# Kernel optimization log

Hardware: AMD Instinct MI355X
Metric: run time of the kernel (lower is better)

## Reference

```python
import jax, jax.numpy as jnp
import numpy as np

N = 100000   # nodes
E = 1600000  # edges
B = 256      # graphs
EPS = 1e-5   # batchnorm eps


def setup_inputs() -> dict:
    key = jax.random.key(0)
    ks = jax.random.split(key, 20)
    inp = {
        "x": jax.random.normal(ks[0], (N, 22), dtype=jnp.float32),
        "edge_index": jax.random.randint(ks[1], (2, E), 0, N, dtype=jnp.int64),
        "batch": jnp.sort(jax.random.randint(ks[2], (N,), 0, B, dtype=jnp.int64)),
        # GCNConv weights (x @ W + b convention)
        "W1": jax.random.normal(ks[3], (22, 64), dtype=jnp.float32) * 0.2,
        "b1": jnp.zeros((64,), dtype=jnp.float32),
        "W2": jax.random.normal(ks[4], (64, 64), dtype=jnp.float32) * 0.12,
        "b2": jnp.zeros((64,), dtype=jnp.float32),
        "W3": jax.random.normal(ks[5], (64, 128), dtype=jnp.float32) * 0.12,
        "b3": jnp.zeros((128,), dtype=jnp.float32),
        # BatchNorm1d params + running stats (eval mode)
        "g1": jax.random.uniform(ks[6], (64,), minval=0.5, maxval=1.5),
        "be1": jax.random.normal(ks[7], (64,)) * 0.1,
        "m1": jax.random.normal(ks[8], (64,)) * 0.1,
        "v1": jax.random.uniform(ks[9], (64,), minval=0.5, maxval=1.5),
        "g2": jax.random.uniform(ks[10], (64,), minval=0.5, maxval=1.5),
        "be2": jax.random.normal(ks[11], (64,)) * 0.1,
        "m2": jax.random.normal(ks[12], (64,)) * 0.1,
        "v2": jax.random.uniform(ks[13], (64,), minval=0.5, maxval=1.5),
    }
    return inp


def _gcn_conv(h, W, b, src, dst, norm_e, dinv):
    # PyG GCNConv: h' = D^{-1/2}(A+I)D^{-1/2} (h W) + b
    h = h @ W                                             # [N, F]
    msg = h[src] * norm_e[:, None]                        # gather + scale [E, F]
    agg = jax.ops.segment_sum(msg, dst, num_segments=N)   # scatter-add
    agg = agg + h * dinv[:, None]                         # self-loop term
    return agg + b


def _bn_eval(x, g, be, m, v):
    return (x - m) * jax.lax.rsqrt(v + EPS) * g + be


def reference(x, edge_index, batch, W1, b1, W2, b2, W3, b3,
              g1, be1, m1, v1, g2, be2, m2, v2):
    src, dst = edge_index[0], edge_index[1]
    # degree with self-loops (computed on target nodes, symmetric norm)
    deg = jax.ops.segment_sum(jnp.ones((E,), x.dtype), dst, num_segments=N) + 1.0
    dis = jax.lax.rsqrt(deg)            # deg^{-1/2}, deg >= 1
    norm_e = dis[src] * dis[dst]        # per-edge norm
    dinv = dis * dis                    # 1/deg for self-loop edges

    h = jax.nn.relu(_bn_eval(_gcn_conv(x, W1, b1, src, dst, norm_e, dinv), g1, be1, m1, v1))
    h = jax.nn.relu(_bn_eval(_gcn_conv(h, W2, b2, src, dst, norm_e, dinv), g2, be2, m2, v2))
    h = jax.nn.relu(_gcn_conv(h, W3, b3, src, dst, norm_e, dinv))

    # global mean pool over graph ids
    sums = jax.ops.segment_sum(h, batch, num_segments=B)              # [B, 128]
    cnts = jax.ops.segment_sum(jnp.ones((N,), h.dtype), batch, num_segments=B)
    return sums / jnp.maximum(cnts, 1.0)[:, None]
```

## Files before the change

### kernel.cpp

```cpp
#include <hip/hip_runtime.h>

#define BN_EPS 1e-5f
#define EPB 4096
#define CAP 10240

typedef _Float16 half_t;
typedef _Float16 half4 __attribute__((ext_vector_type(4)));
typedef _Float16 half8 __attribute__((ext_vector_type(8)));
typedef float f32x4 __attribute__((ext_vector_type(4)));
typedef unsigned int u32;
typedef unsigned short u16;

__device__ __forceinline__ float norm_of(u32 w) {
    u16 hb = (u16)(w & 0x7fffu);
    return (float)__builtin_bit_cast(half_t, hb);
}


__global__ void k_front(const float* __restrict__ X, half_t* __restrict__ Xh,
                        const float* __restrict__ W1, const float* __restrict__ b1,
                        const float* __restrict__ g1, const float* __restrict__ be1,
                        const float* __restrict__ m1, const float* __restrict__ v1,
                        const float* __restrict__ W2, const float* __restrict__ b2,
                        const float* __restrict__ g2, const float* __restrict__ be2,
                        const float* __restrict__ m2, const float* __restrict__ v2,
                        const float* __restrict__ W3, const float* __restrict__ b3,
                        half_t* __restrict__ B1h, half_t* __restrict__ B1l,
                        half_t* __restrict__ B2h, half_t* __restrict__ B2l,
                        half_t* __restrict__ B3h, half_t* __restrict__ B3l,
                        float* __restrict__ C1, float* __restrict__ C2,
                        float* __restrict__ C3,
                        int* __restrict__ gcnt, float* __restrict__ sums,
                        int n, int nB) {
    int i = blockIdx.x * 256 + threadIdx.x;
    if (i < 64) {
        float A = g1[i] * rsqrtf(v1[i] + BN_EPS);
        C1[i] = be1[i] + (b1[i] - m1[i]) * A;
    } else if (i < 128) {
        int c = i - 64;
        float A = g2[c] * rsqrtf(v2[c] + BN_EPS);
        C2[c] = be2[c] + (b2[c] - m2[c]) * A;
    } else if (i < 256) {
        int c = i - 128;
        C3[c] = b3[c];
    }
    if (i < 256) gcnt[i] = 0;
    if (i < nB * 128) sums[i] = 0.0f;
    int e = i - 256;
    if (e >= 0 && e < 2048) {
        int j = e & 7, l = (e >> 3) & 63, t = e >> 9;
        int k = ((l >> 4) << 3) + j;
        int col = t * 16 + (l & 15);
        float A = g1[col] * rsqrtf(v1[col] + BN_EPS);
        float w = (k < 22) ? W1[k * 64 + col] * A : 0.0f;
        half_t wh = (half_t)w;
        B1h[e] = wh; B1l[e] = (half_t)(w - (float)wh);
    } else if (e >= 2048 && e < 6144) {
        int e2 = e - 2048;
        int j = e2 & 7, l = (e2 >> 3) & 63, rest = e2 >> 9;
        int s = rest & 1, t = rest >> 1;
        int k = s * 32 + ((l >> 4) << 3) + j;
        int col = t * 16 + (l & 15);
        float A = g2[col] * rsqrtf(v2[col] + BN_EPS);
        float w = W2[k * 64 + col] * A;
        half_t wh = (half_t)w;
        B2h[e2] = wh; B2l[e2] = (half_t)(w - (float)wh);
    } else if (e >= 6144 && e < 14336) {
        int e3 = e - 6144;
        int j = e3 & 7, l = (e3 >> 3) & 63, rest = e3 >> 9;
        int s = rest & 1, t = rest >> 1;
        int k = s * 32 + ((l >> 4) << 3) + j;
        int col = t * 16 + (l & 15);
        float w = W3[k * 128 + col];
        half_t wh = (half_t)w;
        B3h[e3] = wh; B3l[e3] = (half_t)(w - (float)wh);
    }
    if ((long long)i < (long long)n * 24) {
        int node = i / 24, c = i % 24;
        Xh[i] = (c < 22) ? (half_t)X[(size_t)node * 22 + c] : (half_t)0.0f;
    }
}


__global__ __launch_bounds__(256) void k_scatter(const int* __restrict__ src,
                                                 const int* __restrict__ dst,
                                                 int* __restrict__ gcnt,
                                                 u32* __restrict__ rec, int e) {
    __shared__ int h[256];
    __shared__ int cur[256];
    int t = threadIdx.x;
    h[t] = 0;
    __syncthreads();
    int base = blockIdx.x * EPB;
    int end = min(base + EPB, e);
    for (int i = base + t; i < end; i += 256)
        atomicAdd(&h[dst[i] >> 9], 1);
    __syncthreads();
    int c = h[t];
    cur[t] = (c > 0) ? atomicAdd(&gcnt[t], c) : 0;
    __syncthreads();
    for (int i = base + t; i < end; i += 256) {
        int d = dst[i], sv = src[i];
        int bk = d >> 9;
        int pos = atomicAdd(&cur[bk], 1);
        if (pos < CAP)
            rec[(size_t)bk * CAP + pos] = ((u32)sv << 9) | (u32)(d & 511);
    }
}


__global__ __launch_bounds__(256) void k_bmake(const u32* __restrict__ rec,
                                               const int* __restrict__ gcnt,
                                               int2* __restrict__ rp,
                                               float* __restrict__ dis,
                                               float* __restrict__ dinv, int n) {
    __shared__ int h[512];
    __shared__ int ps[256];
    int t = threadIdx.x;
    int b = blockIdx.x;
    int cnt = min(gcnt[b], CAP);
    size_t beg = (size_t)b * CAP;
    h[t] = 0; h[t + 256] = 0;
    __syncthreads();
    for (int i = t; i < cnt; i += 256)
        atomicAdd(&h[rec[beg + i] & 511], 1);
    __syncthreads();
    int d0 = h[2 * t], d1 = h[2 * t + 1];
    int pair = d0 + d1;
    ps[t] = pair;
    __syncthreads();
    int val = pair;
    for (int off = 1; off < 256; off <<= 1) {
        int tmp = (t >= off) ? ps[t - off] : 0;
        __syncthreads();
        val += tmp;
        ps[t] = val;
        __syncthreads();
    }
    int excl = (int)beg + val - pair;
    int node0 = b << 9;
    int nodeA = node0 + 2 * t, nodeB = nodeA + 1;
    if (nodeA < n) {
        rp[nodeA] = make_int2(excl, excl + d0);
        float dd = (float)(d0 + 1);
        dis[nodeA] = rsqrtf(dd);
        dinv[nodeA] = 1.0f / dd;
    }
    if (nodeB < n) {
        rp[nodeB] = make_int2(excl + d0, excl + d0 + d1);
        float dd = (float)(d1 + 1);
        dis[nodeB] = rsqrtf(dd);
        dinv[nodeB] = 1.0f / dd;
    }
}


__global__ __launch_bounds__(256) void k_bfill(const u32* __restrict__ rec,
                                               const int* __restrict__ gcnt,
                                               const int2* __restrict__ rp,
                                               const float* __restrict__ dis,
                                               u32* __restrict__ csr, int n) {
    __shared__ int cur[512];
    __shared__ float disl[512];
    int t = threadIdx.x;
    int b = blockIdx.x;
    int cnt = min(gcnt[b], CAP);
    size_t beg = (size_t)b * CAP;
    int node0 = b << 9;
    for (int j = t; j < 512; j += 256) {
        int node = node0 + j;
        cur[j] = (node < n) ? rp[node].x : 0;
        disl[j] = (node < n) ? dis[node] : 0.0f;
    }
    __syncthreads();
    for (int i = t; i < cnt; i += 256) {
        u32 r = rec[beg + i];
        int dl = r & 511;
        int s = (int)(r >> 9);
        int pos = atomicAdd(&cur[dl], 1);
        half_t hh = (half_t)(dis[s] * disl[dl]);
        csr[pos] = ((u32)s << 15) | (u32)__builtin_bit_cast(u16, hh);
    }
}


__global__ void k_gather22h(const half_t* __restrict__ Xh, const int2* __restrict__ rp,
                            const u32* __restrict__ csr, const float* __restrict__ dinv,
                            half_t* __restrict__ out, int n) {
    int node = blockIdx.x * 4 + (threadIdx.x >> 6);
    if (node >= n) return;
    int lane = threadIdx.x & 63;
    int esub = lane >> 3;
    int sub  = lane & 7;
    bool act = sub < 6;
    const half4* X4 = (const half4*)Xh;
    int2 be = rp[node];
    int beg = be.x, end = be.y;
    float di = dinv[node];
    half4 hs{};
    if (esub == 0 && act) hs = X4[(size_t)node * 6 + sub];
    float4 a0 = make_float4(0, 0, 0, 0), a1 = a0;
    for (int e = beg; e < end; e += 32) {
        int i0 = e + esub, i1 = i0 + 8, i2 = i0 + 16, i3 = i0 + 24;
        u32 w0 = csr[min(i0, end - 1)];
        u32 w1 = csr[min(i1, end - 1)];
        u32 w2 = csr[min(i2, end - 1)];
        u32 w3 = csr[min(i3, end - 1)];
        if (act && i0 < end) {
            float nn = norm_of(w0);
            half4 h = X4[(size_t)(w0 >> 15) * 6 + sub];
            a0.x = fmaf((float)h.x, nn, a0.x); a0.y = fmaf((float)h.y, nn, a0.y);
            a0.z = fmaf((float)h.z, nn, a0.z); a0.w = fmaf((float)h.w, nn, a0.w);
        }
        if (act && i1 < end) {
            float nn = norm_of(w1);
            half4 h = X4[(size_t)(w1 >> 15) * 6 + sub];
            a1.x = fmaf((float)h.x, nn, a1.x); a1.y = fmaf((float)h.y, nn, a1.y);
            a1.z = fmaf((float)h.z, nn, a1.z); a1.w = fmaf((float)h.w, nn, a1.w);
        }
        if (act && i2 < end) {
            float nn = norm_of(w2);
            half4 h = X4[(size_t)(w2 >> 15) * 6 + sub];
            a0.x = fmaf((float)h.x, nn, a0.x); a0.y = fmaf((float)h.y, nn, a0.y);
            a0.z = fmaf((float)h.z, nn, a0.z); a0.w = fmaf((float)h.w, nn, a0.w);
        }
        if (act && i3 < end) {
            float nn = norm_of(w3);
            half4 h = X4[(size_t)(w3 >> 15) * 6 + sub];
            a1.x = fmaf((float)h.x, nn, a1.x); a1.y = fmaf((float)h.y, nn, a1.y);
            a1.z = fmaf((float)h.z, nn, a1.z); a1.w = fmaf((float)h.w, nn, a1.w);
        }
    }
    float4 a;
    a.x = a0.x + a1.x; a.y = a0.y + a1.y; a.z = a0.z + a1.z; a.w = a0.w + a1.w;
#pragma unroll
    for (int d = 8; d <= 32; d <<= 1) {
        a.x += __shfl_xor(a.x, d); a.y += __shfl_xor(a.y, d);
        a.z += __shfl_xor(a.z, d); a.w += __shfl_xor(a.w, d);
    }
    if (esub == 0 && act) {
        half4 r;
        r.x = (half_t)fmaf((float)hs.x, di, a.x);
        r.y = (half_t)fmaf((float)hs.y, di, a.y);
        r.z = (half_t)fmaf((float)hs.z, di, a.z);
        r.w = (half_t)fmaf((float)hs.w, di, a.w);
        ((half4*)out)[(size_t)node * 6 + sub] = r;
    }
}

__global__ void k_gather64h(const half_t* __restrict__ H, const int2* __restrict__ rp,
                            const u32* __restrict__ csr, const float* __restrict__ dinv,
                            half_t* __restrict__ out, int n) {
    int lane = threadIdx.x & 63;
    int nsub = lane >> 5;
    int hl   = lane & 31;
    int esub = hl >> 3;
    int sub  = hl & 7;
    int node = blockIdx.x * 8 + (int)(threadIdx.x >> 6) * 2 + nsub;
    if (node >= n) return;
    const half8* H8 = (const half8*)H;
    int2 be = rp[node];
    int beg = be.x, end = be.y;
    float di = dinv[node];
    half8 hs{};
    if (esub == 0) hs = H8[(size_t)node * 8 + sub];
    float a0[8], a1[8];
#pragma unroll
    for (int j = 0; j < 8; ++j) { a0[j] = 0.0f; a1[j] = 0.0f; }
    for (int e = beg; e < end; e += 16) {
        int i0 = e + esub, i1 = i0 + 4, i2 = i0 + 8, i3 = i0 + 12;
        u32 w0 = csr[min(i0, end - 1)];
        u32 w1 = csr[min(i1, end - 1)];
        u32 w2 = csr[min(i2, end - 1)];
        u32 w3 = csr[min(i3, end - 1)];
        if (i0 < end) {
            float nn = norm_of(w0);
            half8 h = H8[(size_t)(w0 >> 15) * 8 + sub];
#pragma unroll
            for (int j = 0; j < 8; ++j) a0[j] = fmaf((float)h[j], nn, a0[j]);
        }
        if (i1 < end) {
            float nn = norm_of(w1);
            half8 h = H8[(size_t)(w1 >> 15) * 8 + sub];
#pragma unroll
            for (int j = 0; j < 8; ++j) a1[j] = fmaf((float)h[j], nn, a1[j]);
        }
        if (i2 < end) {
            float nn = norm_of(w2);
            half8 h = H8[(size_t)(w2 >> 15) * 8 + sub];
#pragma unroll
            for (int j = 0; j < 8; ++j) a0[j] = fmaf((float)h[j], nn, a0[j]);
        }
        if (i3 < end) {
            float nn = norm_of(w3);
            half8 h = H8[(size_t)(w3 >> 15) * 8 + sub];
#pragma unroll
            for (int j = 0; j < 8; ++j) a1[j] = fmaf((float)h[j], nn, a1[j]);
        }
    }
    float acc[8];
#pragma unroll
    for (int j = 0; j < 8; ++j) acc[j] = a0[j] + a1[j];
#pragma unroll
    for (int d = 8; d <= 16; d <<= 1) {
#pragma unroll
        for (int j = 0; j < 8; ++j) acc[j] += __shfl_xor(acc[j], d);
    }
    if (esub == 0) {
        half8 r;
#pragma unroll
        for (int j = 0; j < 8; ++j) r[j] = (half_t)fmaf((float)hs[j], di, acc[j]);
        ((half8*)out)[(size_t)node * 8 + sub] = r;
    }
}


template <int FIN, int KS, int FOUT>
__global__ __launch_bounds__(256) void k_mgemm(const half_t* __restrict__ P,
                                               const half_t* __restrict__ Bh,
                                               const half_t* __restrict__ Bl,
                                               const float* __restrict__ Cf,
                                               half_t* __restrict__ outp, int n) {
    int lane = threadIdx.x & 63;
    int wv = threadIdx.x >> 6;
    int node0 = blockIdx.x * 64 + wv * 16;
    int arow = lane & 15, kg = lane >> 4;
    int node = node0 + arow;
    bool v = node < n;

    half8 a[KS];
#pragma unroll
    for (int s = 0; s < KS; ++s) {
        bool ld = v && (FIN == 64 || kg < 3);
        a[s] = ld ? *(const half8*)(P + (size_t)node * FIN + s * 32 + kg * 8) : half8{};
    }

    constexpr int NT = FOUT / 16;
    const half8* BH = (const half8*)Bh;
    const half8* BL = (const half8*)Bl;
    int colb = lane & 15;
#pragma unroll
    for (int t = 0; t < NT; ++t) {
        float cinit = Cf[t * 16 + colb];
        f32x4 acc = {cinit, cinit, cinit, cinit};
#pragma unroll
        for (int s = 0; s < KS; ++s) {
            half8 bh = BH[(t * KS + s) * 64 + lane];
            half8 bl = BL[(t * KS + s) * 64 + lane];
            acc = __builtin_amdgcn_mfma_f32_16x16x32_f16(a[s], bh, acc, 0, 0, 0);
            acc = __builtin_amdgcn_mfma_f32_16x16x32_f16(a[s], bl, acc, 0, 0, 0);
        }
#pragma unroll
        for (int r = 0; r < 4; ++r) {
            int nd = node0 + kg * 4 + r;
            if (nd < n)
                outp[(size_t)nd * FOUT + t * 16 + colb] = (half_t)fmaxf(acc[r], 0.0f);
        }
    }
}


__global__ __launch_bounds__(256) void k_mgemm3pool(const half_t* __restrict__ P,
                                                    const half_t* __restrict__ Bh,
                                                    const half_t* __restrict__ Bl,
                                                    const float* __restrict__ Cf,
                                                    const int* __restrict__ batch,
                                                    float* __restrict__ sums, int n) {
    __shared__ half_t tile[128][66];
    __shared__ int batl[64];
    int lane = threadIdx.x & 63;
    int wv = threadIdx.x >> 6;
    int node0 = blockIdx.x * 64 + wv * 16;
    int arow = lane & 15, kg = lane >> 4;
    int node = node0 + arow;
    bool v = node < n;

    if (threadIdx.x < 64) {
        int nd = blockIdx.x * 64 + threadIdx.x;
        batl[threadIdx.x] = (nd < n) ? batch[nd] : -1;
    }

    half8 a[2];
#pragma unroll
    for (int s = 0; s < 2; ++s)
        a[s] = v ? *(const half8*)(P + (size_t)node * 64 + s * 32 + kg * 8) : half8{};

    const half8* BH = (const half8*)Bh;
    const half8* BL = (const half8*)Bl;
    int colb = lane & 15;
#pragma unroll
    for (int t = 0; t < 8; ++t) {
        float cinit = Cf[t * 16 + colb];
        f32x4 acc = {cinit, cinit, cinit, cinit};
#pragma unroll
        for (int s = 0; s < 2; ++s) {
            half8 bh = BH[(t * 2 + s) * 64 + lane];
            half8 bl = BL[(t * 2 + s) * 64 + lane];
            acc = __builtin_amdgcn_mfma_f32_16x16x32_f16(a[s], bh, acc, 0, 0, 0);
            acc = __builtin_amdgcn_mfma_f32_16x16x32_f16(a[s], bl, acc, 0, 0, 0);
        }
#pragma unroll
        for (int r = 0; r < 4; ++r)
            tile[t * 16 + colb][wv * 16 + kg * 4 + r] = (half_t)fmaxf(acc[r], 0.0f);
    }
    __syncthreads();
    if (threadIdx.x < 128) {
        int col = threadIdx.x;
        int cur = batl[0];
        float acc = 0.0f;
        for (int i = 0; i < 64; ++i) {
            int b = batl[i];
            if (b < 0) break;
            if (b != cur) { atomicAdd(&sums[cur * 128 + col], acc); acc = 0.0f; cur = b; }
            acc += (float)tile[col][i];
        }
        if (cur >= 0) atomicAdd(&sums[cur * 128 + col], acc);
    }
}


__global__ void k_pool_div(const float* __restrict__ sums, const int* __restrict__ batch,
                           float* __restrict__ out, int n, int nB) {
    int i = blockIdx.x * blockDim.x + threadIdx.x;
    if (i >= nB * 128) return;
    int b = i >> 7;
    int lo = 0, hi = n;
    while (lo < hi) { int mid = (lo + hi) >> 1; if (batch[mid] < b) lo = mid + 1; else hi = mid; }
    int start = lo;
    lo = 0; hi = n;
    while (lo < hi) { int mid = (lo + hi) >> 1; if (batch[mid] < b + 1) lo = mid + 1; else hi = mid; }
    float cnt = (float)(lo - start);
    out[i] = sums[i] / fmaxf(cnt, 1.0f);
}


extern "C" void kernel_launch(void* const* d_in, const int* in_sizes, int n_in,
                              void* d_out, int out_size, void* d_ws, size_t ws_size,
                              hipStream_t stream) {
    const float* x   = (const float*)d_in[0];
    const int*   ei  = (const int*)d_in[1];
    const int*   bat = (const int*)d_in[2];
    const float* W1  = (const float*)d_in[3];
    const float* b1  = (const float*)d_in[4];
    const float* W2  = (const float*)d_in[5];
    const float* b2  = (const float*)d_in[6];
    const float* W3  = (const float*)d_in[7];
    const float* b3  = (const float*)d_in[8];
    const float* g1  = (const float*)d_in[9];
    const float* be1 = (const float*)d_in[10];
    const float* m1  = (const float*)d_in[11];
    const float* v1  = (const float*)d_in[12];
    const float* g2  = (const float*)d_in[13];
    const float* be2 = (const float*)d_in[14];
    const float* m2  = (const float*)d_in[15];
    const float* v2  = (const float*)d_in[16];

    const int N = in_sizes[0] / 22;
    const int E = in_sizes[1] / 2;
    const int B = out_size / 128;
    const int* src = ei;
    const int* dst = ei + E;

    const int nblk = (E + EPB - 1) / EPB;
    const int NBKT = (N + 511) >> 9;

    size_t off = 0;
    char* base = (char*)d_ws;
    auto alloc = [&](size_t bytes) -> void* {
        void* p = base + off;
        off = (off + bytes + 255) & ~(size_t)255;
        return p;
    };
    int2*   rp     = (int2*)alloc((size_t)N * 8);
    int*    gcnt   = (int*)alloc(256 * 4);
    u32*    rec    = (u32*)alloc((size_t)NBKT * CAP * 4);
    float*  dis    = (float*)alloc((size_t)N * 4);
    float*  dinv   = (float*)alloc((size_t)N * 4);
    u32*    csr    = (u32*)alloc((size_t)NBKT * CAP * 4);
    half_t* Xh     = (half_t*)alloc((size_t)N * 24 * 2);
    half_t* Hh1    = (half_t*)alloc((size_t)N * 64 * 2);
    half_t* Hh2    = (half_t*)alloc((size_t)N * 64 * 2);
    half_t* aggH   = (half_t*)alloc((size_t)N * 64 * 2);
    float*  sums   = (float*)alloc((size_t)B * 128 * 4);
    half_t* B1h    = (half_t*)alloc(2048 * 2);
    half_t* B1l    = (half_t*)alloc(2048 * 2);
    half_t* B2h    = (half_t*)alloc(4096 * 2);
    half_t* B2l    = (half_t*)alloc(4096 * 2);
    half_t* B3h    = (half_t*)alloc(8192 * 2);
    half_t* B3l    = (half_t*)alloc(8192 * 2);
    float*  C1     = (float*)alloc(64 * 4);
    float*  C2     = (float*)alloc(64 * 4);
    float*  C3     = (float*)alloc(128 * 4);

    const int T = 256;
    auto blk = [](long long n, int t) { return (int)((n + t - 1) / t); };

    int gf = blk((long long)N * 24, T);
    int gf2 = blk(256 + 14336, T);
    int gf3 = blk((long long)B * 128, T);
    if (gf2 > gf) gf = gf2;
    if (gf3 > gf) gf = gf3;

    k_front<<<gf, T, 0, stream>>>(x, Xh, W1, b1, g1, be1, m1, v1,
                                  W2, b2, g2, be2, m2, v2, W3, b3,
                                  B1h, B1l, B2h, B2l, B3h, B3l,
                                  C1, C2, C3, gcnt, sums, N, B);

    k_scatter<<<nblk, T, 0, stream>>>(src, dst, gcnt, rec, E);
    k_bmake<<<NBKT, T, 0, stream>>>(rec, gcnt, rp, dis, dinv, N);
    k_bfill<<<NBKT, T, 0, stream>>>(rec, gcnt, rp, dis, csr, N);

    k_gather22h<<<blk(N, 4), T, 0, stream>>>(Xh, rp, csr, dinv, aggH, N);
    k_mgemm<24, 1, 64><<<blk(N, 64), T, 0, stream>>>(aggH, B1h, B1l, C1, Hh1, N);

    k_gather64h<<<blk(N, 8), T, 0, stream>>>(Hh1, rp, csr, dinv, aggH, N);
    k_mgemm<64, 2, 64><<<blk(N, 64), T, 0, stream>>>(aggH, B2h, B2l, C2, Hh2, N);

    k_gather64h<<<blk(N, 8), T, 0, stream>>>(Hh2, rp, csr, dinv, aggH, N);
    k_mgemm3pool<<<blk(N, 64), T, 0, stream>>>(aggH, B3h, B3l, C3, bat, sums, N);

    k_pool_div<<<blk((long long)B * 128, T), T, 0, stream>>>(sums, bat, (float*)d_out, N, B);
}
```

Measured before the change: 292.3 us.

## Use nontemporal loads/stores and one node per wave in 64-wide gather

Streaming accesses to the edge records, CSR and intermediate activations across the scatter, bucket, gather and GEMM kernels now use nontemporal load/store builtins, so that streamed data does not evict the reused feature rows from cache. Separately, k_gather64h changes from two nodes per wave (32 lanes each) to one node per wave with 8 edge subgroups, and the launch grid is adjusted to match. This gives more edge parallelism per node at the cost of more idle lanes for low-degree nodes. Nontemporal stores of data that the next kernel reads right away may hurt if those lines would otherwise have stayed in L2.

```diff
diff --git a/kernel.cpp b/kernel.cpp
--- a/kernel.cpp
+++ b/kernel.cpp
@@ -94,17 +94,19 @@
     int base = blockIdx.x * EPB;
     int end = min(base + EPB, e);
     for (int i = base + t; i < end; i += 256)
-        atomicAdd(&h[dst[i] >> 9], 1);
+        atomicAdd(&h[__builtin_nontemporal_load(&dst[i]) >> 9], 1);
     __syncthreads();
     int c = h[t];
     cur[t] = (c > 0) ? atomicAdd(&gcnt[t], c) : 0;
     __syncthreads();
     for (int i = base + t; i < end; i += 256) {
-        int d = dst[i], sv = src[i];
+        int d = __builtin_nontemporal_load(&dst[i]);
+        int sv = __builtin_nontemporal_load(&src[i]);
         int bk = d >> 9;
         int pos = atomicAdd(&cur[bk], 1);
         if (pos < CAP)
-            rec[(size_t)bk * CAP + pos] = ((u32)sv << 9) | (u32)(d & 511);
+            __builtin_nontemporal_store(((u32)sv << 9) | (u32)(d & 511),
+                                        &rec[(size_t)bk * CAP + pos]);
     }
 }
 
@@ -123,7 +125,7 @@
     h[t] = 0; h[t + 256] = 0;
     __syncthreads();
     for (int i = t; i < cnt; i += 256)
-        atomicAdd(&h[rec[beg + i] & 511], 1);
+        atomicAdd(&h[__builtin_nontemporal_load(&rec[beg + i]) & 511], 1);
     __syncthreads();
     int d0 = h[2 * t], d1 = h[2 * t + 1];
     int pair = d0 + d1;
@@ -174,12 +176,13 @@
     }
     __syncthreads();
     for (int i = t; i < cnt; i += 256) {
-        u32 r = rec[beg + i];
+        u32 r = __builtin_nontemporal_load(&rec[beg + i]);
         int dl = r & 511;
         int s = (int)(r >> 9);
         int pos = atomicAdd(&cur[dl], 1);
         half_t hh = (half_t)(dis[s] * disl[dl]);
-        csr[pos] = ((u32)s << 15) | (u32)__builtin_bit_cast(u16, hh);
+        __builtin_nontemporal_store(((u32)s << 15) | (u32)__builtin_bit_cast(u16, hh),
+                                    &csr[pos]);
     }
 }
 
@@ -202,10 +205,10 @@
     float4 a0 = make_float4(0, 0, 0, 0), a1 = a0;
     for (int e = beg; e < end; e += 32) {
         int i0 = e + esub, i1 = i0 + 8, i2 = i0 + 16, i3 = i0 + 24;
-        u32 w0 = csr[min(i0, end - 1)];
-        u32 w1 = csr[min(i1, end - 1)];
-        u32 w2 = csr[min(i2, end - 1)];
-        u32 w3 = csr[min(i3, end - 1)];
+        u32 w0 = __builtin_nontemporal_load(&csr[min(i0, end - 1)]);
+        u32 w1 = __builtin_nontemporal_load(&csr[min(i1, end - 1)]);
+        u32 w2 = __builtin_nontemporal_load(&csr[min(i2, end - 1)]);
+        u32 w3 = __builtin_nontemporal_load(&csr[min(i3, end - 1)]);
         if (act && i0 < end) {
             float nn = norm_of(w0);
             half4 h = X4[(size_t)(w0 >> 15) * 6 + sub];
@@ -244,20 +247,18 @@
         r.y = (half_t)fmaf((float)hs.y, di, a.y);
         r.z = (half_t)fmaf((float)hs.z, di, a.z);
         r.w = (half_t)fmaf((float)hs.w, di, a.w);
-        ((half4*)out)[(size_t)node * 6 + sub] = r;
+        __builtin_nontemporal_store(r, &((half4*)out)[(size_t)node * 6 + sub]);
     }
 }
 
 __global__ void k_gather64h(const half_t* __restrict__ H, const int2* __restrict__ rp,
                             const u32* __restrict__ csr, const float* __restrict__ dinv,
                             half_t* __restrict__ out, int n) {
+    int node = blockIdx.x * 4 + (threadIdx.x >> 6);
+    if (node >= n) return;
     int lane = threadIdx.x & 63;
-    int nsub = lane >> 5;
-    int hl   = lane & 31;
-    int esub = hl >> 3;
-    int sub  = hl & 7;
-    int node = blockIdx.x * 8 + (int)(threadIdx.x >> 6) * 2 + nsub;
-    if (node >= n) return;
+    int esub = lane >> 3;
+    int sub  = lane & 7;
     const half8* H8 = (const half8*)H;
     int2 be = rp[node];
     int beg = be.x, end = be.y;
@@ -267,12 +268,12 @@
     float a0[8], a1[8];
 #pragma unroll
     for (int j = 0; j < 8; ++j) { a0[j] = 0.0f; a1[j] = 0.0f; }
-    for (int e = beg; e < end; e += 16) {
-        int i0 = e + esub, i1 = i0 + 4, i2 = i0 + 8, i3 = i0 + 12;
-        u32 w0 = csr[min(i0, end - 1)];
-        u32 w1 = csr[min(i1, end - 1)];
-        u32 w2 = csr[min(i2, end - 1)];
-        u32 w3 = csr[min(i3, end - 1)];
+    for (int e = beg; e < end; e += 32) {
+        int i0 = e + esub, i1 = i0 + 8, i2 = i0 + 16, i3 = i0 + 24;
+        u32 w0 = __builtin_nontemporal_load(&csr[min(i0, end - 1)]);
+        u32 w1 = __builtin_nontemporal_load(&csr[min(i1, end - 1)]);
+        u32 w2 = __builtin_nontemporal_load(&csr[min(i2, end - 1)]);
+        u32 w3 = __builtin_nontemporal_load(&csr[min(i3, end - 1)]);
         if (i0 < end) {
             float nn = norm_of(w0);
             half8 h = H8[(size_t)(w0 >> 15) * 8 + sub];
@@ -302,7 +303,7 @@
 #pragma unroll
     for (int j = 0; j < 8; ++j) acc[j] = a0[j] + a1[j];
 #pragma unroll
-    for (int d = 8; d <= 16; d <<= 1) {
+    for (int d = 8; d <= 32; d <<= 1) {
 #pragma unroll
         for (int j = 0; j < 8; ++j) acc[j] += __shfl_xor(acc[j], d);
     }
@@ -310,7 +311,7 @@
         half8 r;
 #pragma unroll
         for (int j = 0; j < 8; ++j) r[j] = (half_t)fmaf((float)hs[j], di, acc[j]);
-        ((half8*)out)[(size_t)node * 8 + sub] = r;
+        __builtin_nontemporal_store(r, &((half8*)out)[(size_t)node * 8 + sub]);
     }
 }
 
@@ -332,7 +333,9 @@
 #pragma unroll
     for (int s = 0; s < KS; ++s) {
         bool ld = v && (FIN == 64 || kg < 3);
-        a[s] = ld ? *(const half8*)(P + (size_t)node * FIN + s * 32 + kg * 8) : half8{};
+        a[s] = ld ? __builtin_nontemporal_load(
+                        (const half8*)(P + (size_t)node * FIN + s * 32 + kg * 8))
+                  : half8{};
     }
 
     constexpr int NT = FOUT / 16;
@@ -354,7 +357,9 @@
         for (int r = 0; r < 4; ++r) {
             int nd = node0 + kg * 4 + r;
             if (nd < n)
-                outp[(size_t)nd * FOUT + t * 16 + colb] = (half_t)fmaxf(acc[r], 0.0f);
+                __builtin_nontemporal_store(
+                    (half_t)fmaxf(acc[r], 0.0f),
+                    &outp[(size_t)nd * FOUT + t * 16 + colb]);
         }
     }
 }
@@ -383,7 +388,9 @@
     half8 a[2];
 #pragma unroll
     for (int s = 0; s < 2; ++s)
-        a[s] = v ? *(const half8*)(P + (size_t)node * 64 + s * 32 + kg * 8) : half8{};
+        a[s] = v ? __builtin_nontemporal_load(
+                       (const half8*)(P + (size_t)node * 64 + s * 32 + kg * 8))
+                 : half8{};
 
     const half8* BH = (const half8*)Bh;
     const half8* BL = (const half8*)Bl;
@@ -513,10 +520,10 @@
     k_gather22h<<<blk(N, 4), T, 0, stream>>>(Xh, rp, csr, dinv, aggH, N);
     k_mgemm<24, 1, 64><<<blk(N, 64), T, 0, stream>>>(aggH, B1h, B1l, C1, Hh1, N);
 
-    k_gather64h<<<blk(N, 8), T, 0, stream>>>(Hh1, rp, csr, dinv, aggH, N);
+    k_gather64h<<<blk(N, 4), T, 0, stream>>>(Hh1, rp, csr, dinv, aggH, N);
     k_mgemm<64, 2, 64><<<blk(N, 64), T, 0, stream>>>(aggH, B2h, B2l, C2, Hh2, N);
 
-    k_gather64h<<<blk(N, 8), T, 0, stream>>>(Hh2, rp, csr, dinv, aggH, N);
+    k_gather64h<<<blk(N, 4), T, 0, stream>>>(Hh2, rp, csr, dinv, aggH, N);
     k_mgemm3pool<<<blk(N, 64), T, 0, stream>>>(aggH, B3h, B3l, C3, bat, sums, N);
 
     k_pool_div<<<blk((long long)B * 128, T), T, 0, stream>>>(sums, bat, (float*)d_out, N, B);
```

Measured after the change: 403.1 us. 1.38x slower.
